# Kernel optimization log

Hardware: AMD Instinct MI355X
Metric: run time of the kernel (lower is better)

Reference implementation:

```python
import jax, jax.numpy as jnp
import numpy as np

B, T, D, H = 2, 2048, 1024, 16
HD = D // H  # head dim = 64; rope half-dim = 32


def setup_inputs() -> dict:
    key = jax.random.key(0)
    ks = jax.random.split(key, 8)
    x = jax.random.normal(ks[0], (B, T, D), dtype=jnp.float32)
    # additive causal mask (upper triangle = -inf-like), as typically passed in
    mask = jnp.triu(jnp.full((T, T), -1e9, dtype=jnp.float32), k=1)
    # standard RoPE angles: theta = pos / 10000^(2i/hd)
    inv_freq = 1.0 / (10000.0 ** (np.arange(0, HD, 2, dtype=np.float32) / HD))
    ang = np.arange(T, dtype=np.float32)[:, None] * inv_freq[None, :]  # [T, HD//2]
    cos = jnp.asarray(np.cos(ang), dtype=jnp.float32)
    sin = jnp.asarray(np.sin(ang), dtype=jnp.float32)
    s = 1.0 / np.sqrt(D)
    Wq = jax.random.normal(ks[1], (D, D), dtype=jnp.float32) * s
    bq = jnp.zeros((D,), dtype=jnp.float32)
    Wk = jax.random.normal(ks[2], (D, D), dtype=jnp.float32) * s
    Wv = jax.random.normal(ks[3], (D, D), dtype=jnp.float32) * s
    bv = jnp.zeros((D,), dtype=jnp.float32)
    Wo = jax.random.normal(ks[4], (D, D), dtype=jnp.float32) * s
    bo = jnp.zeros((D,), dtype=jnp.float32)
    return {"x": x, "mask": mask, "cos": cos, "sin": sin, "Wq": Wq, "bq": bq,
            "Wk": Wk, "Wv": Wv, "bv": bv, "Wo": Wo, "bo": bo}


def _apply_rope(t, cos, sin):
    # t: [B, T, H, HD]; cos/sin: [T, HD//2]; complex multiply on (even, odd) pairs
    t = t.reshape(B, T, H, HD // 2, 2)
    t0, t1 = t[..., 0], t[..., 1]
    c = cos[None, :, None, :]
    s = sin[None, :, None, :]
    out = jnp.stack([t0 * c - t1 * s, t0 * s + t1 * c], axis=-1)
    return out.reshape(B, T, H, HD)


def reference(x, mask, cos, sin, Wq, bq, Wk, Wv, bv, Wo, bo):
    scale = float(HD) ** (-0.25)
    q = (x @ Wq.T + bq).reshape(B, T, H, HD)
    k = (x @ Wk.T).reshape(B, T, H, HD)  # key proj has no bias
    v = (x @ Wv.T + bv).reshape(B, T, H, HD)
    q = _apply_rope(q, cos, sin)
    k = _apply_rope(k, cos, sin)
    q = q.transpose(0, 2, 1, 3) * scale  # [B,H,T,HD]
    k = k.transpose(0, 2, 1, 3) * scale
    v = v.transpose(0, 2, 1, 3)
    qk = jnp.einsum("bhtd,bhsd->bhts", q, k) + mask  # [B,H,T,T]
    qk = qk.astype(jnp.float32)
    w = jax.nn.softmax(qk, axis=-1).astype(q.dtype)
    wv = jnp.einsum("bhts,bhsd->bhtd", w, v)
    wv = wv.transpose(0, 2, 1, 3).reshape(B, T, D)
    out = wv @ Wo.T + bo
    return out, qk
```

## Files before the change

### kernel.cpp

```cpp
#include <hip/hip_runtime.h>
#include <math.h>

#define Tc 2048
#define Dc 1024
#define Hc 16
#define HDc 64
#define BT 4096
#define SCALE 0.35355339059327379f

typedef _Float16 f16;
typedef __attribute__((ext_vector_type(4))) _Float16 f16x4;
typedef __attribute__((ext_vector_type(8))) _Float16 f16x8;
typedef __attribute__((ext_vector_type(4))) float f32x4;

__device__ __forceinline__ void gload16(const f16* g, f16* l)
{
    __builtin_amdgcn_global_load_lds(
        (const __attribute__((address_space(1))) void*)g,
        (__attribute__((address_space(3))) void*)l, 16, 0, 0);
}

__global__ __launch_bounds__(256)
void cast_kernel(const float* __restrict__ x,
                 const float* __restrict__ Wq, const float* __restrict__ Wk,
                 const float* __restrict__ Wv, const float* __restrict__ Wo,
                 f16* __restrict__ xh,
                 f16* __restrict__ Wqh, f16* __restrict__ Wkh,
                 f16* __restrict__ Wvh, f16* __restrict__ Woh)
{
    const int u = blockIdx.y;
    const float* s; f16* d;
    if (u < 4) { s = x + (size_t)u * (1u << 20); d = xh + (size_t)u * (1u << 20); }
    else switch (u) {
        case 4:  s = Wq; d = Wqh; break;
        case 5:  s = Wk; d = Wkh; break;
        case 6:  s = Wv; d = Wvh; break;
        default: s = Wo; d = Woh; break;
    }
    int i = blockIdx.x * 256 + threadIdx.x;
    float4 v = ((const float4*)s)[i];
    f16x4 o = {(f16)v.x, (f16)v.y, (f16)v.z, (f16)v.w};
    ((f16x4*)d)[i] = o;
}

#define GEMM_BODY(Aptr, Bptr)                                                        \
    __shared__ f16 As[128][64];                                                      \
    __shared__ f16 Bs[128][64];                                                      \
    const int tid = threadIdx.x;                                                     \
    const int w = tid >> 6, l = tid & 63;                                            \
    const int lr = l & 15, lq = l >> 4;                                              \
    const int wr = w >> 1, wc = w & 1;                                               \
    const int m0 = blockIdx.y * 128, n0 = blockIdx.x * 128;                          \
    const int srow8 = l >> 3, sslot = l & 7;                                         \
    f32x4 acc[4][4] = {};                                                            \
    for (int k0 = 0; k0 < Dc; k0 += 64) {                                            \
        __syncthreads();                                                             \
        _Pragma("unroll")                                                            \
        for (int c = 0; c < 4; c++) {                                                \
            int chunk = w * 4 + c;                                                   \
            int row = chunk * 8 + srow8;                                             \
            int col = (sslot ^ (row & 7)) * 8;                                       \
            gload16(&Aptr[(size_t)(m0 + row) * Dc + k0 + col],                       \
                    (f16*)((char*)&As[0][0] + chunk * 1024));                        \
            gload16(&Bptr[(size_t)(n0 + row) * Dc + k0 + col],                       \
                    (f16*)((char*)&Bs[0][0] + chunk * 1024));                        \
        }                                                                            \
        __syncthreads();                                                             \
        _Pragma("unroll")                                                            \
        for (int kk = 0; kk < 2; kk++) {                                             \
            f16x8 af[4], bf[4];                                                      \
            _Pragma("unroll")                                                        \
            for (int mi = 0; mi < 4; mi++) {                                         \
                int row = 64 * wr + 16 * mi + lr;                                    \
                int bo = (lq * 16 + kk * 64) ^ ((row & 7) << 4);                     \
                af[mi] = *(const f16x8*)((const char*)&As[0][0] + row * 128 + bo);   \
            }                                                                        \
            _Pragma("unroll")                                                        \
            for (int ni = 0; ni < 4; ni++) {                                         \
                int row = 64 * wc + 16 * ni + lr;                                    \
                int bo = (lq * 16 + kk * 64) ^ ((row & 7) << 4);                     \
                bf[ni] = *(const f16x8*)((const char*)&Bs[0][0] + row * 128 + bo);   \
            }                                                                        \
            _Pragma("unroll")                                                        \
            for (int mi = 0; mi < 4; mi++)                                           \
                _Pragma("unroll")                                                    \
                for (int ni = 0; ni < 4; ni++)                                       \
                    acc[mi][ni] = __builtin_amdgcn_mfma_f32_16x16x32_f16(            \
                        af[mi], bf[ni], acc[mi][ni], 0, 0, 0);                       \
        }                                                                            \
    }

__global__ __launch_bounds__(256)
void qkv_proj_kernel(const f16* __restrict__ xh,
                     const f16* __restrict__ Wqh, const f16* __restrict__ Wkh,
                     const f16* __restrict__ Wvh,
                     const float* __restrict__ bq, const float* __restrict__ bv,
                     f16* __restrict__ qh, f16* __restrict__ kh, f16* __restrict__ vh,
                     const float* __restrict__ cosp, const float* __restrict__ sinp)
{
    const int mode = blockIdx.z;
    const f16* W = (mode == 0) ? Wqh : (mode == 1 ? Wkh : Wvh);
    const float* bias = (mode == 0) ? bq : (mode == 2 ? bv : nullptr);
    f16* dst = (mode == 0) ? qh : (mode == 1 ? kh : vh);

    GEMM_BODY(xh, W)

    #pragma unroll
    for (int mi = 0; mi < 4; mi++) {
        #pragma unroll
        for (int ni = 0; ni < 4; ni++) {
            #pragma unroll
            for (int i = 0; i < 4; i++) {
                int gm = m0 + 64 * wr + 16 * mi + lq * 4 + i;
                int gn = n0 + 64 * wc + 16 * ni + lr;
                float v = acc[mi][ni][i];
                if (bias) v += bias[gn];
                int b = gm >> 11, t = gm & 2047;
                int h = gn >> 6, d = gn & 63;
                if (mode != 2) {
                    float pv = __shfl_xor(v, 1, 64);
                    int p = d >> 1;
                    float c = cosp[t * 32 + p], s = sinp[t * 32 + p];
                    v = (d & 1) ? (pv * s + v * c) : (v * c - pv * s);
                    v *= SCALE;
                }
                dst[((size_t)(b * Hc + h) * Tc + t) * HDc + d] = (f16)v;
            }
        }
    }
}

__global__ __launch_bounds__(256)
void out_proj_kernel(const f16* __restrict__ A, const f16* __restrict__ W,
                     const float* __restrict__ bias, float* __restrict__ out)
{
    GEMM_BODY(A, W)

    #pragma unroll
    for (int mi = 0; mi < 4; mi++)
        #pragma unroll
        for (int ni = 0; ni < 4; ni++)
            #pragma unroll
            for (int i = 0; i < 4; i++) {
                int gm = m0 + 64 * wr + 16 * mi + lq * 4 + i;
                int gn = n0 + 64 * wc + 16 * ni + lr;
                out[(size_t)gm * Dc + gn] = acc[mi][ni][i] + bias[gn];
            }
}

__global__ __launch_bounds__(256, 6)
void flash_kernel(const f16* __restrict__ qh, const f16* __restrict__ kh,
                  const f16* __restrict__ vh, f16* __restrict__ wvh,
                  float* __restrict__ qk)
{
    const int z = blockIdx.y;
    const int t0 = (gridDim.x - 1 - blockIdx.x) * 64;
    const int tid = threadIdx.x;
    const int w = tid >> 6, l = tid & 63;
    const int lr = l & 15, lq = l >> 4;

    __shared__ f16 Ks[64][64];
    __shared__ f16 VsT[64][68];
    __shared__ f16 Ps[64][68];

    const f16* Qg = qh + (size_t)z * Tc * HDc;
    const f16* Kg = kh + (size_t)z * Tc * HDc;
    const f16* Vg = vh + (size_t)z * Tc * HDc;
    float* C = qk + (size_t)z * Tc * Tc;

    f16x8 aq[2];
    #pragma unroll
    for (int ks = 0; ks < 2; ks++)
        aq[ks] = *(const f16x8*)&Qg[(size_t)(t0 + 16 * w + lr) * HDc + lq * 8 + 32 * ks];

    {
        int r = t0 + (tid >> 2);
        int n4 = (Tc - t0 - 64) >> 2;
        float4 mv; mv.x = mv.y = mv.z = mv.w = -1e9f;
        float4* rowp = (float4*)(C + (size_t)r * Tc + t0 + 64);
        for (int c = (tid & 3); c < n4; c += 4) rowp[c] = mv;
    }

    f32x4 O[4] = {};
    float mrow[4], lrow[4];
    #pragma unroll
    for (int i = 0; i < 4; i++) { mrow[i] = -1e30f; lrow[i] = 0.f; }

    const int srow8 = l >> 3, sslot = l & 7;

    for (int s0 = 0; s0 <= t0; s0 += 64) {
        __syncthreads();

        #pragma unroll
        for (int c = 0; c < 2; c++) {
            int chunk = w * 2 + c;
            int row = chunk * 8 + srow8;
            int col = (sslot ^ (row & 7)) * 8;
            gload16(&Kg[(size_t)(s0 + row) * HDc + col],
                    (f16*)((char*)&Ks[0][0] + chunk * 1024));
        }
        {
            const f16* vp = &Vg[(size_t)(s0 + l) * HDc + w * 16];
            f16x8 v0 = *(const f16x8*)vp;
            f16x8 v1 = *(const f16x8*)(vp + 8);
            #pragma unroll
            for (int j = 0; j < 8; j++) {
                VsT[w * 16 + j][l]     = v0[j];
                VsT[w * 16 + 8 + j][l] = v1[j];
            }
        }
        __syncthreads();

        f32x4 S[4] = {};
        __builtin_amdgcn_s_setprio(1);
        #pragma unroll
        for (int ks = 0; ks < 2; ks++) {
            #pragma unroll
            for (int ni = 0; ni < 4; ni++) {
                int krow = 16 * ni + lr;
                int bo = (lq * 16 + ks * 64) ^ ((krow & 7) << 4);
                f16x8 bk = *(const f16x8*)((const char*)&Ks[0][0] + krow * 128 + bo);
                S[ni] = __builtin_amdgcn_mfma_f32_16x16x32_f16(aq[ks], bk, S[ni], 0, 0, 0);
            }
        }
        __builtin_amdgcn_s_setprio(0);

        if (s0 == t0) {
            #pragma unroll
            for (int ni = 0; ni < 4; ni++)
                #pragma unroll
                for (int i = 0; i < 4; i++) {
                    int tg = t0 + 16 * w + lq * 4 + i;
                    int sg = s0 + 16 * ni + lr;
                    if (sg > tg) S[ni][i] = -1e9f;
                }
        }

        #pragma unroll
        for (int ni = 0; ni < 4; ni++)
            #pragma unroll
            for (int i = 0; i < 4; i++) {
                int tg = t0 + 16 * w + lq * 4 + i;
                int sg = s0 + 16 * ni + lr;
                C[(size_t)tg * Tc + sg] = S[ni][i];
            }

        #pragma unroll
        for (int i = 0; i < 4; i++) {
            float v = fmaxf(fmaxf(S[0][i], S[1][i]), fmaxf(S[2][i], S[3][i]));
            v = fmaxf(v, __shfl_xor(v, 1, 64));
            v = fmaxf(v, __shfl_xor(v, 2, 64));
            v = fmaxf(v, __shfl_xor(v, 4, 64));
            v = fmaxf(v, __shfl_xor(v, 8, 64));
            float mnew = fmaxf(mrow[i], v);
            float alpha = __expf(mrow[i] - mnew);
            mrow[i] = mnew;
            float rs = 0.f;
            #pragma unroll
            for (int ni = 0; ni < 4; ni++) {
                float p = __expf(S[ni][i] - mnew);
                S[ni][i] = p;
                rs += p;
            }
            rs += __shfl_xor(rs, 1, 64);
            rs += __shfl_xor(rs, 2, 64);
            rs += __shfl_xor(rs, 4, 64);
            rs += __shfl_xor(rs, 8, 64);
            lrow[i] = lrow[i] * alpha + rs;
            #pragma unroll
            for (int ni = 0; ni < 4; ni++) O[ni][i] *= alpha;
        }

        #pragma unroll
        for (int ni = 0; ni < 4; ni++)
            #pragma unroll
            for (int i = 0; i < 4; i++)
                Ps[16 * w + lq * 4 + i][16 * ni + lr] = (f16)S[ni][i];

        __builtin_amdgcn_s_setprio(1);
        #pragma unroll
        for (int ks = 0; ks < 2; ks++) {
            f16x8 ap = *(const f16x8*)&Ps[16 * w + lr][lq * 8 + 32 * ks];
            #pragma unroll
            for (int ni = 0; ni < 4; ni++) {
                f16x8 bv = *(const f16x8*)&VsT[16 * ni + lr][lq * 8 + 32 * ks];
                O[ni] = __builtin_amdgcn_mfma_f32_16x16x32_f16(ap, bv, O[ni], 0, 0, 0);
            }
        }
        __builtin_amdgcn_s_setprio(0);
    }

    const int b = z >> 4, h = z & 15;
    #pragma unroll
    for (int ni = 0; ni < 4; ni++)
        #pragma unroll
        for (int i = 0; i < 4; i++) {
            int tg = t0 + 16 * w + lq * 4 + i;
            int d = 16 * ni + lr;
            float o = O[ni][i] / lrow[i];
            wvh[((size_t)(b * Tc + tg)) * Dc + h * HDc + d] = (f16)o;
        }
}

extern "C" void kernel_launch(void* const* d_in, const int* in_sizes, int n_in,
                              void* d_out, int out_size, void* d_ws, size_t ws_size,
                              hipStream_t stream)
{
    const float* x    = (const float*)d_in[0];
    const float* cosp = (const float*)d_in[2];
    const float* sinp = (const float*)d_in[3];
    const float* Wq   = (const float*)d_in[4];
    const float* bq   = (const float*)d_in[5];
    const float* Wk   = (const float*)d_in[6];
    const float* Wv   = (const float*)d_in[7];
    const float* bv   = (const float*)d_in[8];
    const float* Wo   = (const float*)d_in[9];
    const float* bo   = (const float*)d_in[10];

    float* out = (float*)d_out;
    float* qk  = out + (size_t)BT * Dc;

    f16* ws  = (f16*)d_ws;
    f16* xh  = ws;
    f16* Wqh = xh  + (size_t)BT * Dc;
    f16* Wkh = Wqh + (size_t)Dc * Dc;
    f16* Wvh = Wkh + (size_t)Dc * Dc;
    f16* Woh = Wvh + (size_t)Dc * Dc;
    f16* qh  = Woh + (size_t)Dc * Dc;
    f16* kh  = qh  + (size_t)BT * Dc;
    f16* vh  = kh  + (size_t)BT * Dc;
    f16* wvh = vh  + (size_t)BT * Dc;

    dim3 blk(256);

    cast_kernel<<<dim3(1024, 8), blk, 0, stream>>>(
        x, Wq, Wk, Wv, Wo, xh, Wqh, Wkh, Wvh, Woh);

    qkv_proj_kernel<<<dim3(Dc / 128, BT / 128, 3), blk, 0, stream>>>(
        xh, Wqh, Wkh, Wvh, bq, bv, qh, kh, vh, cosp, sinp);

    flash_kernel<<<dim3(Tc / 64, 32), blk, 0, stream>>>(qh, kh, vh, wvh, qk);

    out_proj_kernel<<<dim3(Dc / 128, BT / 128), blk, 0, stream>>>(wvh, Woh, bo, out);
}
```

Baseline: 767.4 us.

## Double-buffer GEMM tiles with 128x64 blocks, DPP row reductions, defer mask fill

The projection GEMMs switch to 128x64 output tiles with double-buffered LDS staging. The next K-slice now loads while MFMAs run on the current one, which also doubles the block count for better CU occupancy, with launch bounds hinting three blocks per CU. In the flash kernel the softmax row max and sum reductions use DPP lane permutes instead of shuffles. The masked-region fill of the qk output moves after the main loop so its stores do not delay the attention compute. The trade-off is more LDS per block and smaller per-block reuse of B.

Result: faster. 726.7 us (-5.3%).

```diff
diff --git a/kernel.cpp b/kernel.cpp
--- a/kernel.cpp
+++ b/kernel.cpp
@@ -18,6 +18,29 @@
     __builtin_amdgcn_global_load_lds(
         (const __attribute__((address_space(1))) void*)g,
         (__attribute__((address_space(3))) void*)l, 16, 0, 0);
+}
+
+template <int C>
+__device__ __forceinline__ float fdpp(float x)
+{
+    return __int_as_float(__builtin_amdgcn_update_dpp(
+        0, __float_as_int(x), C, 0xF, 0xF, true));
+}
+__device__ __forceinline__ float rmax16(float v)
+{
+    v = fmaxf(v, fdpp<0xB1>(v));
+    v = fmaxf(v, fdpp<0x4E>(v));
+    v = fmaxf(v, fdpp<0x124>(v));
+    v = fmaxf(v, fdpp<0x128>(v));
+    return v;
+}
+__device__ __forceinline__ float rsum16(float v)
+{
+    v += fdpp<0xB1>(v);
+    v += fdpp<0x4E>(v);
+    v += fdpp<0x124>(v);
+    v += fdpp<0x128>(v);
+    return v;
 }
 
 __global__ __launch_bounds__(256)
@@ -44,53 +67,63 @@
 }
 
 #define GEMM_BODY(Aptr, Bptr)                                                        \
-    __shared__ f16 As[128][64];                                                      \
-    __shared__ f16 Bs[128][64];                                                      \
+    __shared__ f16 As[2][128 * 64];                                                  \
+    __shared__ f16 Bs[2][64 * 64];                                                   \
     const int tid = threadIdx.x;                                                     \
     const int w = tid >> 6, l = tid & 63;                                            \
     const int lr = l & 15, lq = l >> 4;                                              \
-    const int wr = w >> 1, wc = w & 1;                                               \
-    const int m0 = blockIdx.y * 128, n0 = blockIdx.x * 128;                          \
+    const int m0 = blockIdx.y * 128, n0 = blockIdx.x * 64;                           \
     const int srow8 = l >> 3, sslot = l & 7;                                         \
-    f32x4 acc[4][4] = {};                                                            \
+    f32x4 acc[2][4] = {};                                                            \
+    auto STAGE = [&](int b, int k0) {                                                \
+        _Pragma("unroll")                                                            \
+        for (int c = 0; c < 6; c++) {                                                \
+            int chunk = w * 6 + c;                                                   \
+            if (chunk < 16) {                                                        \
+                int row = chunk * 8 + srow8;                                         \
+                int col = (sslot ^ (row & 7)) * 8;                                   \
+                gload16(&Aptr[(size_t)(m0 + row) * Dc + k0 + col],                   \
+                        &As[b][chunk * 512]);                                        \
+            } else {                                                                 \
+                int row = (chunk - 16) * 8 + srow8;                                  \
+                int col = (sslot ^ (row & 7)) * 8;                                   \
+                gload16(&Bptr[(size_t)(n0 + row) * Dc + k0 + col],                   \
+                        &Bs[b][(chunk - 16) * 512]);                                 \
+            }                                                                        \
+        }                                                                            \
+    };                                                                               \
+    STAGE(0, 0);                                                                     \
+    __syncthreads();                                                                 \
+    int cur = 0;                                                                     \
     for (int k0 = 0; k0 < Dc; k0 += 64) {                                            \
-        __syncthreads();                                                             \
-        _Pragma("unroll")                                                            \
-        for (int c = 0; c < 4; c++) {                                                \
-            int chunk = w * 4 + c;                                                   \
-            int row = chunk * 8 + srow8;                                             \
-            int col = (sslot ^ (row & 7)) * 8;                                       \
-            gload16(&Aptr[(size_t)(m0 + row) * Dc + k0 + col],                       \
-                    (f16*)((char*)&As[0][0] + chunk * 1024));                        \
-            gload16(&Bptr[(size_t)(n0 + row) * Dc + k0 + col],                       \
-                    (f16*)((char*)&Bs[0][0] + chunk * 1024));                        \
-        }                                                                            \
-        __syncthreads();                                                             \
+        if (k0 + 64 < Dc) STAGE(cur ^ 1, k0 + 64);                                   \
         _Pragma("unroll")                                                            \
         for (int kk = 0; kk < 2; kk++) {                                             \
-            f16x8 af[4], bf[4];                                                      \
+            f16x8 af[2], bf[4];                                                      \
             _Pragma("unroll")                                                        \
-            for (int mi = 0; mi < 4; mi++) {                                         \
-                int row = 64 * wr + 16 * mi + lr;                                    \
+            for (int mi = 0; mi < 2; mi++) {                                         \
+                int row = 32 * w + 16 * mi + lr;                                     \
                 int bo = (lq * 16 + kk * 64) ^ ((row & 7) << 4);                     \
-                af[mi] = *(const f16x8*)((const char*)&As[0][0] + row * 128 + bo);   \
+                af[mi] = *(const f16x8*)((const char*)&As[cur][0] + row * 128 + bo); \
             }                                                                        \
             _Pragma("unroll")                                                        \
             for (int ni = 0; ni < 4; ni++) {                                         \
-                int row = 64 * wc + 16 * ni + lr;                                    \
+                int row = 16 * ni + lr;                                              \
                 int bo = (lq * 16 + kk * 64) ^ ((row & 7) << 4);                     \
-                bf[ni] = *(const f16x8*)((const char*)&Bs[0][0] + row * 128 + bo);   \
+                bf[ni] = *(const f16x8*)((const char*)&Bs[cur][0] + row * 128 + bo); \
             }                                                                        \
             _Pragma("unroll")                                                        \
-            for (int mi = 0; mi < 4; mi++)                                           \
+            for (int mi = 0; mi < 2; mi++)                                           \
                 _Pragma("unroll")                                                    \
                 for (int ni = 0; ni < 4; ni++)                                       \
                     acc[mi][ni] = __builtin_amdgcn_mfma_f32_16x16x32_f16(            \
                         af[mi], bf[ni], acc[mi][ni], 0, 0, 0);                       \
         }                                                                            \
-    }
-
-__global__ __launch_bounds__(256)
+        __syncthreads();                                                             \
+        cur ^= 1;                                                                    \
+    }
+
+__global__ __launch_bounds__(256, 3)
 void qkv_proj_kernel(const f16* __restrict__ xh,
                      const f16* __restrict__ Wqh, const f16* __restrict__ Wkh,
                      const f16* __restrict__ Wvh,
@@ -106,13 +139,13 @@
     GEMM_BODY(xh, W)
 
     #pragma unroll
-    for (int mi = 0; mi < 4; mi++) {
+    for (int mi = 0; mi < 2; mi++) {
         #pragma unroll
         for (int ni = 0; ni < 4; ni++) {
             #pragma unroll
             for (int i = 0; i < 4; i++) {
-                int gm = m0 + 64 * wr + 16 * mi + lq * 4 + i;
-                int gn = n0 + 64 * wc + 16 * ni + lr;
+                int gm = m0 + 32 * w + 16 * mi + lq * 4 + i;
+                int gn = n0 + 16 * ni + lr;
                 float v = acc[mi][ni][i];
                 if (bias) v += bias[gn];
                 int b = gm >> 11, t = gm & 2047;
@@ -130,20 +163,20 @@
     }
 }
 
-__global__ __launch_bounds__(256)
+__global__ __launch_bounds__(256, 3)
 void out_proj_kernel(const f16* __restrict__ A, const f16* __restrict__ W,
                      const float* __restrict__ bias, float* __restrict__ out)
 {
     GEMM_BODY(A, W)
 
     #pragma unroll
-    for (int mi = 0; mi < 4; mi++)
+    for (int mi = 0; mi < 2; mi++)
         #pragma unroll
         for (int ni = 0; ni < 4; ni++)
             #pragma unroll
             for (int i = 0; i < 4; i++) {
-                int gm = m0 + 64 * wr + 16 * mi + lq * 4 + i;
-                int gn = n0 + 64 * wc + 16 * ni + lr;
+                int gm = m0 + 32 * w + 16 * mi + lq * 4 + i;
+                int gn = n0 + 16 * ni + lr;
                 out[(size_t)gm * Dc + gn] = acc[mi][ni][i] + bias[gn];
             }
 }
@@ -172,14 +205,6 @@
     #pragma unroll
     for (int ks = 0; ks < 2; ks++)
         aq[ks] = *(const f16x8*)&Qg[(size_t)(t0 + 16 * w + lr) * HDc + lq * 8 + 32 * ks];
-
-    {
-        int r = t0 + (tid >> 2);
-        int n4 = (Tc - t0 - 64) >> 2;
-        float4 mv; mv.x = mv.y = mv.z = mv.w = -1e9f;
-        float4* rowp = (float4*)(C + (size_t)r * Tc + t0 + 64);
-        for (int c = (tid & 3); c < n4; c += 4) rowp[c] = mv;
-    }
 
     f32x4 O[4] = {};
     float mrow[4], lrow[4];
@@ -248,10 +273,7 @@
         #pragma unroll
         for (int i = 0; i < 4; i++) {
             float v = fmaxf(fmaxf(S[0][i], S[1][i]), fmaxf(S[2][i], S[3][i]));
-            v = fmaxf(v, __shfl_xor(v, 1, 64));
-            v = fmaxf(v, __shfl_xor(v, 2, 64));
-            v = fmaxf(v, __shfl_xor(v, 4, 64));
-            v = fmaxf(v, __shfl_xor(v, 8, 64));
+            v = rmax16(v);
             float mnew = fmaxf(mrow[i], v);
             float alpha = __expf(mrow[i] - mnew);
             mrow[i] = mnew;
@@ -262,10 +284,7 @@
                 S[ni][i] = p;
                 rs += p;
             }
-            rs += __shfl_xor(rs, 1, 64);
-            rs += __shfl_xor(rs, 2, 64);
-            rs += __shfl_xor(rs, 4, 64);
-            rs += __shfl_xor(rs, 8, 64);
+            rs = rsum16(rs);
             lrow[i] = lrow[i] * alpha + rs;
             #pragma unroll
             for (int ni = 0; ni < 4; ni++) O[ni][i] *= alpha;
@@ -300,6 +319,14 @@
             float o = O[ni][i] / lrow[i];
             wvh[((size_t)(b * Tc + tg)) * Dc + h * HDc + d] = (f16)o;
         }
+
+    {
+        int r = t0 + (tid >> 2);
+        int n4 = (Tc - t0 - 64) >> 2;
+        float4 mv; mv.x = mv.y = mv.z = mv.w = -1e9f;
+        float4* rowp = (float4*)(C + (size_t)r * Tc + t0 + 64);
+        for (int c = (tid & 3); c < n4; c += 4) rowp[c] = mv;
+    }
 }
 
 extern "C" void kernel_launch(void* const* d_in, const int* in_sizes, int n_in,
@@ -336,10 +363,10 @@
     cast_kernel<<<dim3(1024, 8), blk, 0, stream>>>(
         x, Wq, Wk, Wv, Wo, xh, Wqh, Wkh, Wvh, Woh);
 
-    qkv_proj_kernel<<<dim3(Dc / 128, BT / 128, 3), blk, 0, stream>>>(
+    qkv_proj_kernel<<<dim3(Dc / 64, BT / 128, 3), blk, 0, stream>>>(
         xh, Wqh, Wkh, Wvh, bq, bv, qh, kh, vh, cosp, sinp);
 
     flash_kernel<<<dim3(Tc / 64, 32), blk, 0, stream>>>(qh, kh, vh, wvh, qk);
 
-    out_proj_kernel<<<dim3(Dc / 128, BT / 128), blk, 0, stream>>>(wvh, Woh, bo, out);
-}
+    out_proj_kernel<<<dim3(Dc / 64, BT / 128), blk, 0, stream>>>(wvh, Woh, bo, out);
+}
```
